# Performance work log

Hardware: AMD Instinct MI355X
Metric: run time of the kernel (lower is better)

## Reference

```python
import jax, jax.numpy as jnp
import numpy as np

NUM_EXPERTS = 8
TOP_K = 2


def setup_inputs() -> dict:
    key = jax.random.key(0)
    ks = jax.random.split(key, 5)
    B, S, D, F, E = 4, 2048, 1024, 3584, NUM_EXPERTS
    scale = 0.02
    return {
        "hidden_states": jax.random.normal(ks[0], (B, S, D), dtype=jnp.float32),
        "gate_w": jax.random.normal(ks[1], (E, D), dtype=jnp.float32) * scale,
        "w1": jax.random.normal(ks[2], (E, D, F), dtype=jnp.float32) * scale,
        "w3": jax.random.normal(ks[3], (E, D, F), dtype=jnp.float32) * scale,
        "w2": jax.random.normal(ks[4], (E, F, D), dtype=jnp.float32) * scale,
    }


def reference(hidden_states, gate_w, w1, w3, w2):
    B, S, D = hidden_states.shape
    E = gate_w.shape[0]
    x = hidden_states.reshape(-1, D)  # [T, D]

    # Router: logits -> softmax -> top-k -> renormalize
    router_logits = x @ gate_w.T  # [T, E]
    routing_probs = jax.nn.softmax(router_logits, axis=-1)
    top_w, top_idx = jax.lax.top_k(routing_probs, TOP_K)  # [T, K]
    top_w = top_w / jnp.sum(top_w, axis=-1, keepdims=True)

    # Per-token weight for each expert (0 if not selected): [T, E]
    expert_weight = jnp.sum(
        jax.nn.one_hot(top_idx, E, dtype=x.dtype) * top_w[..., None], axis=1
    )

    # Dense masked dispatch: small fixed loop over experts (E=8), SwiGLU MLP.
    out = jnp.zeros_like(x)
    for e in range(E):
        h = jax.nn.silu(x @ w1[e]) * (x @ w3[e])  # [T, F]
        out = out + expert_weight[:, e:e + 1] * (h @ w2[e])  # [T, D]

    return out.reshape(B, S, D), router_logits
```

## Files before the change

### kernel.cpp

```cpp
#include <hip/hip_runtime.h>
#include <stdint.h>

#define T_TOKENS 8192
#define DDIM 1024
#define FDIM 3584
#define NEXP 8

#define BM 128
#define BK 64
#define MAXTT 136

typedef _Float16 f16x8 __attribute__((ext_vector_type(8)));
typedef float f32x4 __attribute__((ext_vector_type(4)));

__device__ __forceinline__ void gload16(const void* g, void* l) {
  __builtin_amdgcn_global_load_lds(
      (const __attribute__((address_space(1))) void*)g,
      (__attribute__((address_space(3))) void*)l, 16, 0, 0);
}

__global__ __launch_bounds__(256) void router_kernel(
    const float* __restrict__ x, const float* __restrict__ gw,
    float* __restrict__ logits_out, int* __restrict__ counts,
    int* __restrict__ tok_idx, float* __restrict__ tok_w,
    int2* __restrict__ tok_ref, _Float16* __restrict__ xh) {
  int t = blockIdx.x * 4 + (threadIdx.x >> 6);
  int lane = threadIdx.x & 63;
  const float* xr = x + (size_t)t * DDIM;
  float acc[NEXP];
#pragma unroll
  for (int e = 0; e < NEXP; e++) acc[e] = 0.f;
  for (int c = 0; c < DDIM / 64; c++) {
    float xv = xr[c * 64 + lane];
    xh[(size_t)t * DDIM + c * 64 + lane] = (_Float16)xv;
#pragma unroll
    for (int e = 0; e < NEXP; e++) acc[e] += xv * gw[e * DDIM + c * 64 + lane];
  }
#pragma unroll
  for (int e = 0; e < NEXP; e++) {
    for (int off = 32; off > 0; off >>= 1) acc[e] += __shfl_xor(acc[e], off, 64);
  }
  if (lane == 0) {
    float m = acc[0];
    for (int e = 1; e < NEXP; e++) m = fmaxf(m, acc[e]);
    float p[NEXP];
    for (int e = 0; e < NEXP; e++) p[e] = expf(acc[e] - m);
    int e1 = 0;
    for (int e = 1; e < NEXP; e++) if (p[e] > p[e1]) e1 = e;
    int e2 = (e1 == 0) ? 1 : 0;
    for (int e = 0; e < NEXP; e++) { if (e == e1) continue; if (p[e] > p[e2]) e2 = e; }
    float wsum = p[e1] + p[e2];
    float w1v = p[e1] / wsum, w2v = p[e2] / wsum;
    for (int e = 0; e < NEXP; e++) logits_out[(size_t)t * NEXP + e] = acc[e];
    int pos1 = atomicAdd(&counts[e1], 1);
    tok_idx[e1 * T_TOKENS + pos1] = t; tok_w[e1 * T_TOKENS + pos1] = w1v;
    int pos2 = atomicAdd(&counts[e2], 1);
    tok_idx[e2 * T_TOKENS + pos2] = t; tok_w[e2 * T_TOKENS + pos2] = w2v;
    tok_ref[t] = make_int2((e1 << 13) | pos1, (e2 << 13) | pos2);
  }
}

__global__ void prefix_kernel(const int* __restrict__ counts, int* __restrict__ offsets,
                              int* __restrict__ sched) {
  if (threadIdx.x == 0) {
    int s = 0, nt = 0;
    for (int e = 0; e < NEXP; e++) {
      offsets[e] = s;
      int c = counts[e];
      int ntile = (c + BM - 1) / BM;
      for (int i = 0; i < ntile; i++) sched[nt++] = (e << 16) | i;
      s += c;
    }
    offsets[NEXP] = s;
    for (; nt < MAXTT; nt++) sched[nt] = -1;
  }
}

__global__ __launch_bounds__(256) void transpose_f16_kernel(
    const float* __restrict__ in, _Float16* __restrict__ out, int R, int C) {
  __shared__ _Float16 lt[64][72];
  size_t esz = (size_t)R * C;
  in += (size_t)blockIdx.z * esz;
  out += (size_t)blockIdx.z * esz;
  int r0 = blockIdx.y * 64, c0 = blockIdx.x * 64;
  int t = threadIdx.x;
  int r = t & 63, q = t >> 6;
  const float* src = in + (size_t)(r0 + r) * C + c0 + q * 16;
  float4 v0 = ((const float4*)src)[0];
  float4 v1 = ((const float4*)src)[1];
  float4 v2 = ((const float4*)src)[2];
  float4 v3 = ((const float4*)src)[3];
  _Float16 f[16] = {
      (_Float16)v0.x, (_Float16)v0.y, (_Float16)v0.z, (_Float16)v0.w,
      (_Float16)v1.x, (_Float16)v1.y, (_Float16)v1.z, (_Float16)v1.w,
      (_Float16)v2.x, (_Float16)v2.y, (_Float16)v2.z, (_Float16)v2.w,
      (_Float16)v3.x, (_Float16)v3.y, (_Float16)v3.z, (_Float16)v3.w};
#pragma unroll
  for (int j = 0; j < 16; j++) lt[q * 16 + j][r] = f[j];
  __syncthreads();
  _Float16* dst = out + (size_t)(c0 + r) * R + r0 + q * 16;
  *(f16x8*)dst       = *(const f16x8*)&lt[r][q * 16];
  *(f16x8*)(dst + 8) = *(const f16x8*)&lt[r][q * 16 + 8];
}

__global__ __launch_bounds__(256) void gemm1_kernel(
    const _Float16* __restrict__ xh, const _Float16* __restrict__ w1t,
    const _Float16* __restrict__ w3t, const int* __restrict__ counts,
    const int* __restrict__ offsets, const int* __restrict__ tok_idx,
    const int* __restrict__ sched, _Float16* __restrict__ h) {
  int sc = sched[blockIdx.y];
  if (sc < 0) return;
  int e = sc >> 16, rt = sc & 0xFFFF;
  int cnt = counts[e];
  int ct = blockIdx.x;
  int off = offsets[e];

  __shared__ _Float16 lA[BM * 64];
  __shared__ _Float16 lB1[64 * 64];
  __shared__ _Float16 lB3[64 * 64];

  int tid = threadIdx.x, lane = tid & 63, w = tid >> 6;
  int p = lane & 7;
  int rsub = lane >> 3;
  int c = p ^ rsub;

  const _Float16* aG[4];
  _Float16* aL[4];
#pragma unroll
  for (int g = 0; g < 4; g++) {
    int r = w * 32 + g * 8 + rsub;
    int ir = rt * BM + r;
    if (ir >= cnt) ir = cnt - 1;
    int tok = tok_idx[e * T_TOKENS + ir];
    aG[g] = xh + (size_t)tok * DDIM + c * 8;
    aL[g] = lA + (w * 32 + g * 8) * 64;
  }
  const _Float16 *b1G[2], *b3G[2];
  _Float16 *b1L[2], *b3L[2];
#pragma unroll
  for (int g = 0; g < 2; g++) {
    int n = w * 16 + g * 8 + rsub;
    size_t row = (size_t)e * FDIM + (size_t)ct * 64 + n;
    b1G[g] = w1t + row * DDIM + c * 8;
    b3G[g] = w3t + row * DDIM + c * 8;
    b1L[g] = lB1 + (w * 16 + g * 8) * 64;
    b3L[g] = lB3 + (w * 16 + g * 8) * 64;
  }

  f32x4 acc1[2][4], acc3[2][4];
  f32x4 zero = {0.f, 0.f, 0.f, 0.f};
#pragma unroll
  for (int i = 0; i < 2; i++)
#pragma unroll
    for (int j = 0; j < 4; j++) { acc1[i][j] = zero; acc3[i][j] = zero; }

  int wm = w * 32;
  int l15 = lane & 15;
  int qv = lane >> 4;
  int x7 = l15 & 7;

  for (int kt = 0; kt < DDIM / BK; kt++) {
#pragma unroll
    for (int g = 0; g < 4; g++) { gload16(aG[g], aL[g]); aG[g] += 64; }
#pragma unroll
    for (int g = 0; g < 2; g++) {
      gload16(b1G[g], b1L[g]); b1G[g] += 64;
      gload16(b3G[g], b3L[g]); b3G[g] += 64;
    }
    __syncthreads();
#pragma unroll
    for (int kk = 0; kk < 2; kk++) {
      int pc = (kk * 4 + qv) ^ x7;
      f16x8 af[2], b1f[4], b3f[4];
#pragma unroll
      for (int i = 0; i < 2; i++)
        af[i] = *(const f16x8*)&lA[(wm + i * 16 + l15) * 64 + pc * 8];
#pragma unroll
      for (int j = 0; j < 4; j++) {
        b1f[j] = *(const f16x8*)&lB1[(j * 16 + l15) * 64 + pc * 8];
        b3f[j] = *(const f16x8*)&lB3[(j * 16 + l15) * 64 + pc * 8];
      }
#pragma unroll
      for (int i = 0; i < 2; i++)
#pragma unroll
        for (int j = 0; j < 4; j++) {
          acc1[i][j] = __builtin_amdgcn_mfma_f32_16x16x32_f16(af[i], b1f[j], acc1[i][j], 0, 0, 0);
          acc3[i][j] = __builtin_amdgcn_mfma_f32_16x16x32_f16(af[i], b3f[j], acc3[i][j], 0, 0, 0);
        }
    }
    __syncthreads();
  }
  int q4 = qv * 4;
#pragma unroll
  for (int i = 0; i < 2; i++) {
#pragma unroll
    for (int r = 0; r < 4; r++) {
      int row = rt * BM + wm + i * 16 + q4 + r;
      if (row >= cnt) continue;
      _Float16* hrow = h + (size_t)(off + row) * FDIM + (size_t)ct * 64;
#pragma unroll
      for (int j = 0; j < 4; j++) {
        float a = acc1[i][j][r];
        float b = acc3[i][j][r];
        float hv = (a / (1.f + __expf(-a))) * b;
        hrow[j * 16 + l15] = (_Float16)hv;
      }
    }
  }
}

__global__ __launch_bounds__(256) void gemm2_kernel(
    const _Float16* __restrict__ h, const _Float16* __restrict__ w2t,
    const int* __restrict__ counts, const int* __restrict__ offsets,
    const float* __restrict__ tok_w, const int* __restrict__ sched,
    _Float16* __restrict__ part) {
  int sc = sched[blockIdx.y];
  if (sc < 0) return;
  int e = sc >> 16, rt = sc & 0xFFFF;
  int cnt = counts[e];
  int ct = blockIdx.x;
  int off = offsets[e];

  __shared__ _Float16 lA[BM * 64];
  __shared__ _Float16 lB[128 * 64];

  int tid = threadIdx.x, lane = tid & 63, w = tid >> 6;
  int p = lane & 7;
  int rsub = lane >> 3;
  int c = p ^ rsub;

  const _Float16 *aG[4], *bG[4];
  _Float16 *aL[4], *bL[4];
#pragma unroll
  for (int g = 0; g < 4; g++) {
    int r = w * 32 + g * 8 + rsub;
    aG[g] = h + (size_t)(off + rt * BM + r) * FDIM + c * 8;
    aL[g] = lA + (w * 32 + g * 8) * 64;
    size_t row = (size_t)e * DDIM + (size_t)ct * 128 + r;
    bG[g] = w2t + row * FDIM + c * 8;
    bL[g] = lB + (w * 32 + g * 8) * 64;
  }

  f32x4 acc[2][8];
  f32x4 zero = {0.f, 0.f, 0.f, 0.f};
#pragma unroll
  for (int i = 0; i < 2; i++)
#pragma unroll
    for (int j = 0; j < 8; j++) acc[i][j] = zero;

  int wm = w * 32;
  int l15 = lane & 15;
  int qv = lane >> 4;
  int x7 = l15 & 7;

  for (int kt = 0; kt < FDIM / BK; kt++) {
#pragma unroll
    for (int g = 0; g < 4; g++) {
      gload16(aG[g], aL[g]); aG[g] += 64;
      gload16(bG[g], bL[g]); bG[g] += 64;
    }
    __syncthreads();
#pragma unroll
    for (int kk = 0; kk < 2; kk++) {
      int pc = (kk * 4 + qv) ^ x7;
      f16x8 af[2], bf[8];
#pragma unroll
      for (int i = 0; i < 2; i++)
        af[i] = *(const f16x8*)&lA[(wm + i * 16 + l15) * 64 + pc * 8];
#pragma unroll
      for (int j = 0; j < 8; j++)
        bf[j] = *(const f16x8*)&lB[(j * 16 + l15) * 64 + pc * 8];
#pragma unroll
      for (int i = 0; i < 2; i++)
#pragma unroll
        for (int j = 0; j < 8; j++)
          acc[i][j] = __builtin_amdgcn_mfma_f32_16x16x32_f16(af[i], bf[j], acc[i][j], 0, 0, 0);
    }
    __syncthreads();
  }
  int q4 = qv * 4;
#pragma unroll
  for (int i = 0; i < 2; i++) {
#pragma unroll
    for (int r = 0; r < 4; r++) {
      int row = rt * BM + wm + i * 16 + q4 + r;
      if (row >= cnt) continue;
      float wgt = tok_w[e * T_TOKENS + row];
      _Float16* prow = part + (size_t)(off + row) * DDIM + (size_t)ct * 128;
#pragma unroll
      for (int j = 0; j < 8; j++)
        prow[j * 16 + l15] = (_Float16)(acc[i][j][r] * wgt);
    }
  }
}

__global__ __launch_bounds__(256) void gather_kernel(
    const _Float16* __restrict__ part, const int2* __restrict__ tok_ref,
    const int* __restrict__ offsets, float* __restrict__ out) {
  int i = blockIdx.x * 256 + threadIdx.x;
  int t = i >> 7;
  int dc = (i & 127) * 8;
  int2 ref = tok_ref[t];
  int sa = offsets[ref.x >> 13] + (ref.x & 8191);
  int sb = offsets[ref.y >> 13] + (ref.y & 8191);
  f16x8 pa = *(const f16x8*)(part + (size_t)sa * DDIM + dc);
  f16x8 pb = *(const f16x8*)(part + (size_t)sb * DDIM + dc);
  float* dst = out + (size_t)t * DDIM + dc;
#pragma unroll
  for (int j = 0; j < 8; j++) dst[j] = (float)pa[j] + (float)pb[j];
}

extern "C" void kernel_launch(void* const* d_in, const int* in_sizes, int n_in,
                              void* d_out, int out_size, void* d_ws, size_t ws_size,
                              hipStream_t stream) {
  const float* x  = (const float*)d_in[0];
  const float* gw = (const float*)d_in[1];
  const float* w1 = (const float*)d_in[2];
  const float* w3 = (const float*)d_in[3];
  const float* w2 = (const float*)d_in[4];
  float* out = (float*)d_out;
  float* logits = out + (size_t)T_TOKENS * DDIM;

  char* ws = (char*)d_ws;
  const size_t MB = 1024 * 1024;
  int* counts  = (int*)ws;
  int* offsets = (int*)(ws + 64);
  int* sched   = (int*)(ws + 128);
  int* tok_idx = (int*)(ws + 1024);
  float* tok_w = (float*)(ws + 1024 + 262144);
  int2* tok_ref = (int2*)(ws + 1024 + 2 * 262144);
  _Float16* xh  = (_Float16*)(ws + 1 * MB);
  _Float16* w1t = (_Float16*)(ws + 17 * MB);
  _Float16* w3t = (_Float16*)(ws + 73 * MB);
  _Float16* w2t = (_Float16*)(ws + 129 * MB);
  _Float16* h   = (_Float16*)(ws + 185 * MB);
  _Float16* part = (_Float16*)(ws + 304 * MB);

  hipMemsetAsync(counts, 0, 256, stream);

  router_kernel<<<T_TOKENS / 4, 256, 0, stream>>>(x, gw, logits, counts, tok_idx, tok_w, tok_ref, xh);
  prefix_kernel<<<1, 64, 0, stream>>>(counts, offsets, sched);

  transpose_f16_kernel<<<dim3(FDIM / 64, DDIM / 64, NEXP), 256, 0, stream>>>(w1, w1t, DDIM, FDIM);
  transpose_f16_kernel<<<dim3(FDIM / 64, DDIM / 64, NEXP), 256, 0, stream>>>(w3, w3t, DDIM, FDIM);
  transpose_f16_kernel<<<dim3(DDIM / 64, FDIM / 64, NEXP), 256, 0, stream>>>(w2, w2t, FDIM, DDIM);

  gemm1_kernel<<<dim3(FDIM / 64, MAXTT), 256, 0, stream>>>(xh, w1t, w3t, counts, offsets, tok_idx, sched, h);
  gemm2_kernel<<<dim3(DDIM / 128, MAXTT), 256, 0, stream>>>(h, w2t, counts, offsets, tok_w, sched, part);
  gather_kernel<<<T_TOKENS * DDIM / 8 / 256, 256, 0, stream>>>(part, tok_ref, offsets, out);
}
```

Measured before the change: 1.139 ms.

## Double-buffer expert GEMMs with async LDS prefetch and larger per-wave tiles

Both expert GEMMs now use double-buffered LDS, prefetching two K-steps ahead with explicit vmcnt waits and raw barriers, so global-to-LDS loads overlap MFMA work. gemm1 moves to 512-thread blocks with 256x128 tiles and its own tile schedule; gemm2 gives each wave a 64x64 tile instead of 32x128. MFMA sections are wrapped in setprio. This is meant to hide memory latency and raise reuse per LDS load, at the cost of more LDS and registers per block, which may reduce occupancy.

```diff
diff --git a/kernel.cpp b/kernel.cpp
--- a/kernel.cpp
+++ b/kernel.cpp
@@ -6,9 +6,8 @@
 #define FDIM 3584
 #define NEXP 8
 
-#define BM 128
-#define BK 64
-#define MAXTT 136
+#define MAXT1 72
+#define MAXT2 136
 
 typedef _Float16 f16x8 __attribute__((ext_vector_type(8)));
 typedef float f32x4 __attribute__((ext_vector_type(4)));
@@ -61,18 +60,21 @@
 }
 
 __global__ void prefix_kernel(const int* __restrict__ counts, int* __restrict__ offsets,
-                              int* __restrict__ sched) {
+                              int* __restrict__ sched1, int* __restrict__ sched2) {
   if (threadIdx.x == 0) {
-    int s = 0, nt = 0;
+    int s = 0, n1 = 0, n2 = 0;
     for (int e = 0; e < NEXP; e++) {
       offsets[e] = s;
-      int c = counts[e];
-      int ntile = (c + BM - 1) / BM;
-      for (int i = 0; i < ntile; i++) sched[nt++] = (e << 16) | i;
-      s += c;
+      int cc = counts[e];
+      int nt1 = (cc + 255) / 256;
+      for (int i = 0; i < nt1; i++) sched1[n1++] = (e << 16) | i;
+      int nt2 = (cc + 127) / 128;
+      for (int i = 0; i < nt2; i++) sched2[n2++] = (e << 16) | i;
+      s += cc;
     }
     offsets[NEXP] = s;
-    for (; nt < MAXTT; nt++) sched[nt] = -1;
+    for (; n1 < MAXT1; n1++) sched1[n1] = -1;
+    for (; n2 < MAXT2; n2++) sched2[n2] = -1;
   }
 }
 
@@ -103,7 +105,7 @@
   *(f16x8*)(dst + 8) = *(const f16x8*)&lt[r][q * 16 + 8];
 }
 
-__global__ __launch_bounds__(256) void gemm1_kernel(
+__global__ __launch_bounds__(512, 2) void gemm1_kernel(
     const _Float16* __restrict__ xh, const _Float16* __restrict__ w1t,
     const _Float16* __restrict__ w3t, const int* __restrict__ counts,
     const int* __restrict__ offsets, const int* __restrict__ tok_idx,
@@ -115,89 +117,104 @@
   int ct = blockIdx.x;
   int off = offsets[e];
 
-  __shared__ _Float16 lA[BM * 64];
-  __shared__ _Float16 lB1[64 * 64];
-  __shared__ _Float16 lB3[64 * 64];
-
-  int tid = threadIdx.x, lane = tid & 63, w = tid >> 6;
-  int p = lane & 7;
-  int rsub = lane >> 3;
-  int c = p ^ rsub;
-
-  const _Float16* aG[4];
-  _Float16* aL[4];
+  __shared__ _Float16 lds[2][32768];
+
+  int tid = threadIdx.x, lane = tid & 63, wv = tid >> 6;
+  int p = lane & 7, rsub = lane >> 3, c = p ^ rsub;
+
+  const _Float16* aSrc[4];
 #pragma unroll
   for (int g = 0; g < 4; g++) {
-    int r = w * 32 + g * 8 + rsub;
-    int ir = rt * BM + r;
+    int r = wv * 32 + g * 8 + rsub;
+    int ir = rt * 256 + r;
     if (ir >= cnt) ir = cnt - 1;
     int tok = tok_idx[e * T_TOKENS + ir];
-    aG[g] = xh + (size_t)tok * DDIM + c * 8;
-    aL[g] = lA + (w * 32 + g * 8) * 64;
-  }
-  const _Float16 *b1G[2], *b3G[2];
-  _Float16 *b1L[2], *b3L[2];
+    aSrc[g] = xh + (size_t)tok * DDIM + c * 8;
+  }
+  const _Float16 *b1Src[2], *b3Src[2];
 #pragma unroll
   for (int g = 0; g < 2; g++) {
-    int n = w * 16 + g * 8 + rsub;
-    size_t row = (size_t)e * FDIM + (size_t)ct * 64 + n;
-    b1G[g] = w1t + row * DDIM + c * 8;
-    b3G[g] = w3t + row * DDIM + c * 8;
-    b1L[g] = lB1 + (w * 16 + g * 8) * 64;
-    b3L[g] = lB3 + (w * 16 + g * 8) * 64;
-  }
-
-  f32x4 acc1[2][4], acc3[2][4];
+    int n = wv * 16 + g * 8 + rsub;
+    size_t row = (size_t)e * FDIM + (size_t)ct * 128 + n;
+    b1Src[g] = w1t + row * DDIM + c * 8;
+    b3Src[g] = w3t + row * DDIM + c * 8;
+  }
+  int aBase = wv * 2048;
+  int bBase = wv * 1024;
+
+#define G1_ISSUE(t) do { _Float16* Lb = lds[(t) & 1];            \
+    gload16(aSrc[0] + (t) * 64, Lb + aBase);                     \
+    gload16(aSrc[1] + (t) * 64, Lb + aBase + 512);               \
+    gload16(aSrc[2] + (t) * 64, Lb + aBase + 1024);              \
+    gload16(aSrc[3] + (t) * 64, Lb + aBase + 1536);              \
+    gload16(b1Src[0] + (t) * 64, Lb + 16384 + bBase);            \
+    gload16(b1Src[1] + (t) * 64, Lb + 16384 + bBase + 512);      \
+    gload16(b3Src[0] + (t) * 64, Lb + 24576 + bBase);            \
+    gload16(b3Src[1] + (t) * 64, Lb + 24576 + bBase + 512);      \
+  } while (0)
+
+  f32x4 acc1[4][4], acc3[4][4];
   f32x4 zero = {0.f, 0.f, 0.f, 0.f};
 #pragma unroll
-  for (int i = 0; i < 2; i++)
+  for (int i = 0; i < 4; i++)
 #pragma unroll
     for (int j = 0; j < 4; j++) { acc1[i][j] = zero; acc3[i][j] = zero; }
 
-  int wm = w * 32;
-  int l15 = lane & 15;
-  int qv = lane >> 4;
-  int x7 = l15 & 7;
-
-  for (int kt = 0; kt < DDIM / BK; kt++) {
-#pragma unroll
-    for (int g = 0; g < 4; g++) { gload16(aG[g], aL[g]); aG[g] += 64; }
-#pragma unroll
-    for (int g = 0; g < 2; g++) {
-      gload16(b1G[g], b1L[g]); b1G[g] += 64;
-      gload16(b3G[g], b3L[g]); b3G[g] += 64;
-    }
-    __syncthreads();
+  int l15 = lane & 15, qv = lane >> 4, x7 = l15 & 7;
+  int wm = (wv >> 1) * 64, wn = (wv & 1) * 64;
+
+  G1_ISSUE(0);
+  G1_ISSUE(1);
+  for (int t = 0; t < DDIM / 64; t++) {
+    if (t < DDIM / 64 - 1) asm volatile("s_waitcnt vmcnt(8)" ::: "memory");
+    else                   asm volatile("s_waitcnt vmcnt(0)" ::: "memory");
+    __builtin_amdgcn_s_barrier();
+    asm volatile("" ::: "memory");
+    __builtin_amdgcn_sched_barrier(0);
+    const _Float16* L = lds[t & 1];
 #pragma unroll
     for (int kk = 0; kk < 2; kk++) {
       int pc = (kk * 4 + qv) ^ x7;
-      f16x8 af[2], b1f[4], b3f[4];
-#pragma unroll
-      for (int i = 0; i < 2; i++)
-        af[i] = *(const f16x8*)&lA[(wm + i * 16 + l15) * 64 + pc * 8];
-#pragma unroll
-      for (int j = 0; j < 4; j++) {
-        b1f[j] = *(const f16x8*)&lB1[(j * 16 + l15) * 64 + pc * 8];
-        b3f[j] = *(const f16x8*)&lB3[(j * 16 + l15) * 64 + pc * 8];
-      }
-#pragma unroll
-      for (int i = 0; i < 2; i++)
-#pragma unroll
-        for (int j = 0; j < 4; j++) {
+      f16x8 af[4], b1f[4];
+#pragma unroll
+      for (int i = 0; i < 4; i++)
+        af[i] = *(const f16x8*)&L[(wm + i * 16 + l15) * 64 + pc * 8];
+#pragma unroll
+      for (int j = 0; j < 4; j++)
+        b1f[j] = *(const f16x8*)&L[16384 + (wn + j * 16 + l15) * 64 + pc * 8];
+      __builtin_amdgcn_s_setprio(1);
+#pragma unroll
+      for (int i = 0; i < 4; i++)
+#pragma unroll
+        for (int j = 0; j < 4; j++)
           acc1[i][j] = __builtin_amdgcn_mfma_f32_16x16x32_f16(af[i], b1f[j], acc1[i][j], 0, 0, 0);
+      __builtin_amdgcn_s_setprio(0);
+      f16x8 b3f[4];
+#pragma unroll
+      for (int j = 0; j < 4; j++)
+        b3f[j] = *(const f16x8*)&L[24576 + (wn + j * 16 + l15) * 64 + pc * 8];
+      __builtin_amdgcn_s_setprio(1);
+#pragma unroll
+      for (int i = 0; i < 4; i++)
+#pragma unroll
+        for (int j = 0; j < 4; j++)
           acc3[i][j] = __builtin_amdgcn_mfma_f32_16x16x32_f16(af[i], b3f[j], acc3[i][j], 0, 0, 0);
-        }
-    }
-    __syncthreads();
-  }
+      __builtin_amdgcn_s_setprio(0);
+    }
+    __builtin_amdgcn_s_barrier();
+    asm volatile("" ::: "memory");
+    if (t + 2 < DDIM / 64) { G1_ISSUE(t + 2); }
+  }
+#undef G1_ISSUE
+
   int q4 = qv * 4;
 #pragma unroll
-  for (int i = 0; i < 2; i++) {
+  for (int i = 0; i < 4; i++) {
 #pragma unroll
     for (int r = 0; r < 4; r++) {
-      int row = rt * BM + wm + i * 16 + q4 + r;
+      int row = rt * 256 + wm + i * 16 + q4 + r;
       if (row >= cnt) continue;
-      _Float16* hrow = h + (size_t)(off + row) * FDIM + (size_t)ct * 64;
+      _Float16* hrow = h + (size_t)(off + row) * FDIM + (size_t)ct * 128 + wn;
 #pragma unroll
       for (int j = 0; j < 4; j++) {
         float a = acc1[i][j][r];
@@ -209,7 +226,7 @@
   }
 }
 
-__global__ __launch_bounds__(256) void gemm2_kernel(
+__global__ __launch_bounds__(256, 2) void gemm2_kernel(
     const _Float16* __restrict__ h, const _Float16* __restrict__ w2t,
     const int* __restrict__ counts, const int* __restrict__ offsets,
     const float* __restrict__ tok_w, const int* __restrict__ sched,
@@ -221,74 +238,85 @@
   int ct = blockIdx.x;
   int off = offsets[e];
 
-  __shared__ _Float16 lA[BM * 64];
-  __shared__ _Float16 lB[128 * 64];
-
-  int tid = threadIdx.x, lane = tid & 63, w = tid >> 6;
-  int p = lane & 7;
-  int rsub = lane >> 3;
-  int c = p ^ rsub;
-
-  const _Float16 *aG[4], *bG[4];
-  _Float16 *aL[4], *bL[4];
+  __shared__ _Float16 lds[2][16384];
+
+  int tid = threadIdx.x, lane = tid & 63, wv = tid >> 6;
+  int p = lane & 7, rsub = lane >> 3, c = p ^ rsub;
+
+  const _Float16 *aSrc[4], *bSrc[4];
 #pragma unroll
   for (int g = 0; g < 4; g++) {
-    int r = w * 32 + g * 8 + rsub;
-    aG[g] = h + (size_t)(off + rt * BM + r) * FDIM + c * 8;
-    aL[g] = lA + (w * 32 + g * 8) * 64;
-    size_t row = (size_t)e * DDIM + (size_t)ct * 128 + r;
-    bG[g] = w2t + row * FDIM + c * 8;
-    bL[g] = lB + (w * 32 + g * 8) * 64;
-  }
-
-  f32x4 acc[2][8];
+    int r = wv * 32 + g * 8 + rsub;
+    aSrc[g] = h + (size_t)(off + rt * 128 + r) * FDIM + c * 8;
+    bSrc[g] = w2t + ((size_t)e * DDIM + (size_t)ct * 128 + r) * FDIM + c * 8;
+  }
+  int abBase = wv * 2048;
+
+#define G2_ISSUE(t) do { _Float16* Lb = lds[(t) & 1];            \
+    gload16(aSrc[0] + (t) * 64, Lb + abBase);                    \
+    gload16(aSrc[1] + (t) * 64, Lb + abBase + 512);              \
+    gload16(aSrc[2] + (t) * 64, Lb + abBase + 1024);             \
+    gload16(aSrc[3] + (t) * 64, Lb + abBase + 1536);             \
+    gload16(bSrc[0] + (t) * 64, Lb + 8192 + abBase);             \
+    gload16(bSrc[1] + (t) * 64, Lb + 8192 + abBase + 512);       \
+    gload16(bSrc[2] + (t) * 64, Lb + 8192 + abBase + 1024);      \
+    gload16(bSrc[3] + (t) * 64, Lb + 8192 + abBase + 1536);      \
+  } while (0)
+
+  f32x4 acc[4][4];
   f32x4 zero = {0.f, 0.f, 0.f, 0.f};
 #pragma unroll
-  for (int i = 0; i < 2; i++)
-#pragma unroll
-    for (int j = 0; j < 8; j++) acc[i][j] = zero;
-
-  int wm = w * 32;
-  int l15 = lane & 15;
-  int qv = lane >> 4;
-  int x7 = l15 & 7;
-
-  for (int kt = 0; kt < FDIM / BK; kt++) {
-#pragma unroll
-    for (int g = 0; g < 4; g++) {
-      gload16(aG[g], aL[g]); aG[g] += 64;
-      gload16(bG[g], bL[g]); bG[g] += 64;
-    }
-    __syncthreads();
+  for (int i = 0; i < 4; i++)
+#pragma unroll
+    for (int j = 0; j < 4; j++) acc[i][j] = zero;
+
+  int l15 = lane & 15, qv = lane >> 4, x7 = l15 & 7;
+  int wm = (wv >> 1) * 64, wn = (wv & 1) * 64;
+
+  G2_ISSUE(0);
+  G2_ISSUE(1);
+  for (int t = 0; t < FDIM / 64; t++) {
+    if (t < FDIM / 64 - 1) asm volatile("s_waitcnt vmcnt(8)" ::: "memory");
+    else                   asm volatile("s_waitcnt vmcnt(0)" ::: "memory");
+    __builtin_amdgcn_s_barrier();
+    asm volatile("" ::: "memory");
+    __builtin_amdgcn_sched_barrier(0);
+    const _Float16* L = lds[t & 1];
 #pragma unroll
     for (int kk = 0; kk < 2; kk++) {
       int pc = (kk * 4 + qv) ^ x7;
-      f16x8 af[2], bf[8];
-#pragma unroll
-      for (int i = 0; i < 2; i++)
-        af[i] = *(const f16x8*)&lA[(wm + i * 16 + l15) * 64 + pc * 8];
-#pragma unroll
-      for (int j = 0; j < 8; j++)
-        bf[j] = *(const f16x8*)&lB[(j * 16 + l15) * 64 + pc * 8];
-#pragma unroll
-      for (int i = 0; i < 2; i++)
-#pragma unroll
-        for (int j = 0; j < 8; j++)
+      f16x8 af[4], bf[4];
+#pragma unroll
+      for (int i = 0; i < 4; i++)
+        af[i] = *(const f16x8*)&L[(wm + i * 16 + l15) * 64 + pc * 8];
+#pragma unroll
+      for (int j = 0; j < 4; j++)
+        bf[j] = *(const f16x8*)&L[8192 + (wn + j * 16 + l15) * 64 + pc * 8];
+      __builtin_amdgcn_s_setprio(1);
+#pragma unroll
+      for (int i = 0; i < 4; i++)
+#pragma unroll
+        for (int j = 0; j < 4; j++)
           acc[i][j] = __builtin_amdgcn_mfma_f32_16x16x32_f16(af[i], bf[j], acc[i][j], 0, 0, 0);
-    }
-    __syncthreads();
-  }
+      __builtin_amdgcn_s_setprio(0);
+    }
+    __builtin_amdgcn_s_barrier();
+    asm volatile("" ::: "memory");
+    if (t + 2 < FDIM / 64) { G2_ISSUE(t + 2); }
+  }
+#undef G2_ISSUE
+
   int q4 = qv * 4;
 #pragma unroll
-  for (int i = 0; i < 2; i++) {
+  for (int i = 0; i < 4; i++) {
 #pragma unroll
     for (int r = 0; r < 4; r++) {
-      int row = rt * BM + wm + i * 16 + q4 + r;
+      int row = rt * 128 + wm + i * 16 + q4 + r;
       if (row >= cnt) continue;
       float wgt = tok_w[e * T_TOKENS + row];
-      _Float16* prow = part + (size_t)(off + row) * DDIM + (size_t)ct * 128;
-#pragma unroll
-      for (int j = 0; j < 8; j++)
+      _Float16* prow = part + (size_t)(off + row) * DDIM + (size_t)ct * 128 + wn;
+#pragma unroll
+      for (int j = 0; j < 4; j++)
         prow[j * 16 + l15] = (_Float16)(acc[i][j][r] * wgt);
     }
   }
@@ -325,10 +353,11 @@
   const size_t MB = 1024 * 1024;
   int* counts  = (int*)ws;
   int* offsets = (int*)(ws + 64);
-  int* sched   = (int*)(ws + 128);
-  int* tok_idx = (int*)(ws + 1024);
-  float* tok_w = (float*)(ws + 1024 + 262144);
-  int2* tok_ref = (int2*)(ws + 1024 + 2 * 262144);
+  int* sched1  = (int*)(ws + 128);
+  int* sched2  = (int*)(ws + 512);
+  int* tok_idx = (int*)(ws + 2048);
+  float* tok_w = (float*)(ws + 2048 + 262144);
+  int2* tok_ref = (int2*)(ws + 2048 + 2 * 262144);
   _Float16* xh  = (_Float16*)(ws + 1 * MB);
   _Float16* w1t = (_Float16*)(ws + 17 * MB);
   _Float16* w3t = (_Float16*)(ws + 73 * MB);
@@ -339,13 +368,13 @@
   hipMemsetAsync(counts, 0, 256, stream);
 
   router_kernel<<<T_TOKENS / 4, 256, 0, stream>>>(x, gw, logits, counts, tok_idx, tok_w, tok_ref, xh);
-  prefix_kernel<<<1, 64, 0, stream>>>(counts, offsets, sched);
+  prefix_kernel<<<1, 64, 0, stream>>>(counts, offsets, sched1, sched2);
 
   transpose_f16_kernel<<<dim3(FDIM / 64, DDIM / 64, NEXP), 256, 0, stream>>>(w1, w1t, DDIM, FDIM);
   transpose_f16_kernel<<<dim3(FDIM / 64, DDIM / 64, NEXP), 256, 0, stream>>>(w3, w3t, DDIM, FDIM);
   transpose_f16_kernel<<<dim3(DDIM / 64, FDIM / 64, NEXP), 256, 0, stream>>>(w2, w2t, FDIM, DDIM);
 
-  gemm1_kernel<<<dim3(FDIM / 64, MAXTT), 256, 0, stream>>>(xh, w1t, w3t, counts, offsets, tok_idx, sched, h);
-  gemm2_kernel<<<dim3(DDIM / 128, MAXTT), 256, 0, stream>>>(h, w2t, counts, offsets, tok_w, sched, part);
+  gemm1_kernel<<<dim3(FDIM / 128, MAXT1), 512, 0, stream>>>(xh, w1t, w3t, counts, offsets, tok_idx, sched1, h);
+  gemm2_kernel<<<dim3(DDIM / 128, MAXT2), 256, 0, stream>>>(h, w2t, counts, offsets, tok_w, sched2, part);
   gather_kernel<<<T_TOKENS * DDIM / 8 / 256, 256, 0, stream>>>(part, tok_ref, offsets, out);
 }
```

New measurement: 1.034 ms. 1.1x faster.
